# Kernel tuning notes

Measured on AMD Instinct MI355X. Metric: run time of the kernel, lower is better.

The kernel has to match this reference:

```python
import jax, jax.numpy as jnp
import numpy as np

B, CIN, COUT, H, W = 16, 512, 128, 64, 64


def setup_inputs() -> dict:
    key = jax.random.key(0)
    k1, k2, k3 = jax.random.split(key, 3)
    x = jax.random.normal(k1, (B, CIN, H, W), dtype=jnp.float32)
    style = jax.random.normal(k2, (B, CIN), dtype=jnp.float32)
    # kaiming_normal_ on [COUT, CIN, 1, 1]: fan_in = CIN*1*1, std = sqrt(2/fan_in)
    weight = jax.random.normal(k3, (COUT, CIN), dtype=jnp.float32) * np.float32(np.sqrt(2.0 / CIN))
    return {"x": x, "style": style, "weight": weight}


def reference(x, style, weight):
    # Per-sample modulated weight: mw[b,o,c] = style[b,c] * weight[o,c]
    # 1x1 conv, padding=0, stride=1 -> batched channel-mixing GEMM:
    # out[b,o,h,w] = sum_c mw[b,o,c] * x[b,c,h,w]
    return jnp.einsum('oc,bc,bchw->bohw', weight, style, x)
```

## Files before the change

### kernel.cpp

```cpp
#include <hip/hip_runtime.h>
#include <stdint.h>

#define NB    16
#define CIN   512
#define COUT  128
#define HW    4096
#define BN    128
#define BK    32
#define NIT   (CIN / BK)

using bf16x8  = __attribute__((ext_vector_type(8))) __bf16;
using floatx4 = __attribute__((ext_vector_type(4))) float;

__device__ __forceinline__ unsigned short f2bf_bits(float f) {
    union { float f; unsigned u; } v; v.f = f;
    return (unsigned short)((v.u + 0x7fffu + ((v.u >> 16) & 1u)) >> 16);
}

#define GLD16(g, l)                                                            \
    __builtin_amdgcn_global_load_lds(                                          \
        (const __attribute__((address_space(1))) void*)(g),                    \
        (__attribute__((address_space(3))) void*)(l), 16, 0, 0)

__global__ __launch_bounds__(256)
void modw_kernel(const float* __restrict__ style,
                 const float* __restrict__ weight,
                 __bf16* __restrict__ mw)
{
    const int id = blockIdx.x * 256 + threadIdx.x;
    const int k8 = id & 63;
    const int m  = (id >> 6) & 127;
    const int b  = id >> 13;

    const float4 w0 = *(const float4*)(weight + m * CIN + k8 * 8);
    const float4 w1 = *(const float4*)(weight + m * CIN + k8 * 8 + 4);
    const float4 s0 = *(const float4*)(style + b * CIN + k8 * 8);
    const float4 s1 = *(const float4*)(style + b * CIN + k8 * 8 + 4);

    union { unsigned short us[8]; bf16x8 v; } pk;
    pk.us[0] = f2bf_bits(w0.x * s0.x);
    pk.us[1] = f2bf_bits(w0.y * s0.y);
    pk.us[2] = f2bf_bits(w0.z * s0.z);
    pk.us[3] = f2bf_bits(w0.w * s0.w);
    pk.us[4] = f2bf_bits(w1.x * s1.x);
    pk.us[5] = f2bf_bits(w1.y * s1.y);
    pk.us[6] = f2bf_bits(w1.z * s1.z);
    pk.us[7] = f2bf_bits(w1.w * s1.w);
    *(bf16x8*)(mw + ((size_t)(b * 64 + k8) * 128 + m) * 8) = pk.v;
}

__global__ __launch_bounds__(512, 4)
void modconv1x1_kernel(const float* __restrict__ x,
                       const __bf16* __restrict__ mw,
                       float* __restrict__ out)
{
    __shared__ __align__(16) __bf16 Alds[2][4096];
    __shared__ __align__(16) __bf16 Bfs[2][4 * 128 * 8];

    const int tid  = threadIdx.x;
    const int lane = tid & 63;
    const int wave = tid >> 6;
    const int quad = lane >> 4;
    const int l15  = lane & 15;

    const int b  = blockIdx.x >> 5;
    const int n0 = (blockIdx.x & 31) * BN;

    float*       outb = out + (size_t)b * COUT * HW + n0;
    const char*  mwb  = (const char*)mw + (size_t)b * (64 * 128 * 16);

    const int wm = (wave & 1) * 64;
    const int wn = (wave >> 1) * 32;

    const int kg = tid >> 7;
    const int bn = tid & 127;
    const float* xbn = x + (size_t)b * CIN * HW + (size_t)kg * 8 * HW + n0 + bn;

    floatx4 acc[4][2];
    #pragma unroll
    for (int i = 0; i < 4; ++i)
        #pragma unroll
        for (int j = 0; j < 2; ++j)
            acc[i][j] = (floatx4){0.f, 0.f, 0.f, 0.f};

#define SISSUE(T, XR)                                                          \
    {                                                                          \
        const float* xp = xbn + (size_t)(T) * BK * HW;                         \
        _Pragma("unroll")                                                      \
        for (int j = 0; j < 8; ++j) XR[j] = xp[(size_t)j * HW];                \
    }

#define SWRITE(T, XR)                                                          \
    {                                                                          \
        union { unsigned short us[8]; bf16x8 v; } pk;                          \
        _Pragma("unroll")                                                      \
        for (int j = 0; j < 8; ++j) pk.us[j] = f2bf_bits(XR[j]);               \
        *(bf16x8*)&Bfs[(T) & 1][(kg * 128 + bn) * 8] = pk.v;                   \
    }

#define ADMA(T)                                                                \
    {                                                                          \
        const char* at = mwb + (size_t)(T) * 8192;                             \
        GLD16(at + wave * 1024 + lane * 16,                                    \
              (char*)&Alds[(T) & 1][0] + wave * 1024);                        \
    }

#define COMPUTE(BUF)                                                           \
    {                                                                          \
        bf16x8 af[4];                                                          \
        _Pragma("unroll")                                                      \
        for (int tm = 0; tm < 4; ++tm)                                         \
            af[tm] = *(const bf16x8*)&Alds[BUF][(quad * 128 + wm + tm * 16 + l15) * 8]; \
        bf16x8 bfr[2];                                                         \
        _Pragma("unroll")                                                      \
        for (int tn = 0; tn < 2; ++tn)                                         \
            bfr[tn] = *(const bf16x8*)&Bfs[BUF][(quad * 128 + wn + tn * 16 + l15) * 8]; \
        _Pragma("unroll")                                                      \
        for (int tm = 0; tm < 4; ++tm)                                         \
            _Pragma("unroll")                                                  \
            for (int tn = 0; tn < 2; ++tn)                                     \
                acc[tm][tn] = __builtin_amdgcn_mfma_f32_16x16x32_bf16(         \
                    af[tm], bfr[tn], acc[tm][tn], 0, 0, 0);                    \
    }

#define BODYF(IT, XC, XN)                                                      \
    {                                                                          \
        ADMA((IT) + 1)                                                         \
        COMPUTE((IT) & 1)                                                      \
        SISSUE((IT) + 2, XN)                                                   \
        SWRITE((IT) + 1, XC)                                                   \
        asm volatile("s_waitcnt vmcnt(8) lgkmcnt(0)" ::: "memory");            \
        __builtin_amdgcn_s_barrier();                                          \
    }

    float xa[8], xb[8];

    SISSUE(0, xa)
    ADMA(0)
    SWRITE(0, xa)
    SISSUE(1, xb)
    asm volatile("s_waitcnt vmcnt(8) lgkmcnt(0)" ::: "memory");
    __builtin_amdgcn_s_barrier();

    #pragma unroll 1
    for (int it2 = 0; it2 < 7; ++it2) {
        const int it = it2 * 2;
        BODYF(it,     xb, xa)
        BODYF(it + 1, xa, xb)
    }
    {
        ADMA(15)
        COMPUTE(0)
        SWRITE(15, xb)
        asm volatile("s_waitcnt vmcnt(0) lgkmcnt(0)" ::: "memory");
        __builtin_amdgcn_s_barrier();
    }
    COMPUTE(1)

#undef BODYF
#undef COMPUTE
#undef ADMA
#undef SWRITE
#undef SISSUE

    #pragma unroll
    for (int tm = 0; tm < 4; ++tm) {
        const int o = wm + tm * 16 + quad * 4;
        #pragma unroll
        for (int tn = 0; tn < 2; ++tn) {
            const int n = wn + tn * 16 + l15;
            #pragma unroll
            for (int r = 0; r < 4; ++r)
                outb[(size_t)(o + r) * HW + n] = acc[tm][tn][r];
        }
    }
}

extern "C" void kernel_launch(void* const* d_in, const int* in_sizes, int n_in,
                              void* d_out, int out_size, void* d_ws, size_t ws_size,
                              hipStream_t stream) {
    const float* x      = (const float*)d_in[0];
    const float* style  = (const float*)d_in[1];
    const float* weight = (const float*)d_in[2];
    float* out = (float*)d_out;
    __bf16* mw = (__bf16*)d_ws;

    modw_kernel<<<dim3(512), dim3(256), 0, stream>>>(style, weight, mw);
    modconv1x1_kernel<<<dim3(NB * 32), dim3(512), 0, stream>>>(x, mw, out);
}
```

Baseline: 205.8 us.

## Fuse style modulation into GEMM kernel, build A fragments in registers

```diff
diff --git a/kernel.cpp b/kernel.cpp
--- a/kernel.cpp
+++ b/kernel.cpp
@@ -17,44 +17,12 @@
     return (unsigned short)((v.u + 0x7fffu + ((v.u >> 16) & 1u)) >> 16);
 }
 
-#define GLD16(g, l)                                                            \
-    __builtin_amdgcn_global_load_lds(                                          \
-        (const __attribute__((address_space(1))) void*)(g),                    \
-        (__attribute__((address_space(3))) void*)(l), 16, 0, 0)
-
-__global__ __launch_bounds__(256)
-void modw_kernel(const float* __restrict__ style,
-                 const float* __restrict__ weight,
-                 __bf16* __restrict__ mw)
+__global__ __launch_bounds__(512, 4)
+void modconv_fused_kernel(const float* __restrict__ x,
+                          const float* __restrict__ style,
+                          const float* __restrict__ weight,
+                          float* __restrict__ out)
 {
-    const int id = blockIdx.x * 256 + threadIdx.x;
-    const int k8 = id & 63;
-    const int m  = (id >> 6) & 127;
-    const int b  = id >> 13;
-
-    const float4 w0 = *(const float4*)(weight + m * CIN + k8 * 8);
-    const float4 w1 = *(const float4*)(weight + m * CIN + k8 * 8 + 4);
-    const float4 s0 = *(const float4*)(style + b * CIN + k8 * 8);
-    const float4 s1 = *(const float4*)(style + b * CIN + k8 * 8 + 4);
-
-    union { unsigned short us[8]; bf16x8 v; } pk;
-    pk.us[0] = f2bf_bits(w0.x * s0.x);
-    pk.us[1] = f2bf_bits(w0.y * s0.y);
-    pk.us[2] = f2bf_bits(w0.z * s0.z);
-    pk.us[3] = f2bf_bits(w0.w * s0.w);
-    pk.us[4] = f2bf_bits(w1.x * s1.x);
-    pk.us[5] = f2bf_bits(w1.y * s1.y);
-    pk.us[6] = f2bf_bits(w1.z * s1.z);
-    pk.us[7] = f2bf_bits(w1.w * s1.w);
-    *(bf16x8*)(mw + ((size_t)(b * 64 + k8) * 128 + m) * 8) = pk.v;
-}
-
-__global__ __launch_bounds__(512, 4)
-void modconv1x1_kernel(const float* __restrict__ x,
-                       const __bf16* __restrict__ mw,
-                       float* __restrict__ out)
-{
-    __shared__ __align__(16) __bf16 Alds[2][4096];
     __shared__ __align__(16) __bf16 Bfs[2][4 * 128 * 8];
 
     const int tid  = threadIdx.x;
@@ -66,11 +34,16 @@
     const int b  = blockIdx.x >> 5;
     const int n0 = (blockIdx.x & 31) * BN;
 
-    float*       outb = out + (size_t)b * COUT * HW + n0;
-    const char*  mwb  = (const char*)mw + (size_t)b * (64 * 128 * 16);
+    float* outb = out + (size_t)b * COUT * HW + n0;
 
     const int wm = (wave & 1) * 64;
     const int wn = (wave >> 1) * 32;
+
+    const float* wr0 = weight + (size_t)(wm + 0 * 16 + l15) * CIN + quad * 8;
+    const float* wr1 = weight + (size_t)(wm + 1 * 16 + l15) * CIN + quad * 8;
+    const float* wr2 = weight + (size_t)(wm + 2 * 16 + l15) * CIN + quad * 8;
+    const float* wr3 = weight + (size_t)(wm + 3 * 16 + l15) * CIN + quad * 8;
+    const float* sb  = style + (size_t)b * CIN + quad * 8;
 
     const int kg = tid >> 7;
     const int bn = tid & 127;
@@ -82,6 +55,42 @@
         #pragma unroll
         for (int j = 0; j < 2; ++j)
             acc[i][j] = (floatx4){0.f, 0.f, 0.f, 0.f};
+
+    float4 sv0, sv1, w00, w01, w10, w11, w20, w21, w30, w31;
+    bf16x8 af0, af1, af2, af3;
+    float xa[8], xb[8];
+
+#define WLOAD(T)                                                               \
+    {                                                                          \
+        const int ko = (T) * BK;                                               \
+        sv0 = *(const float4*)(sb + ko);  sv1 = *(const float4*)(sb + ko + 4); \
+        w00 = *(const float4*)(wr0 + ko); w01 = *(const float4*)(wr0 + ko + 4);\
+        w10 = *(const float4*)(wr1 + ko); w11 = *(const float4*)(wr1 + ko + 4);\
+        w20 = *(const float4*)(wr2 + ko); w21 = *(const float4*)(wr2 + ko + 4);\
+        w30 = *(const float4*)(wr3 + ko); w31 = *(const float4*)(wr3 + ko + 4);\
+    }
+
+#define ABUILD()                                                               \
+    {                                                                          \
+        union { unsigned short us[8]; bf16x8 v; } p0, p1, p2, p3;              \
+        p0.us[0] = f2bf_bits(w00.x * sv0.x); p0.us[1] = f2bf_bits(w00.y * sv0.y); \
+        p0.us[2] = f2bf_bits(w00.z * sv0.z); p0.us[3] = f2bf_bits(w00.w * sv0.w); \
+        p0.us[4] = f2bf_bits(w01.x * sv1.x); p0.us[5] = f2bf_bits(w01.y * sv1.y); \
+        p0.us[6] = f2bf_bits(w01.z * sv1.z); p0.us[7] = f2bf_bits(w01.w * sv1.w); \
+        p1.us[0] = f2bf_bits(w10.x * sv0.x); p1.us[1] = f2bf_bits(w10.y * sv0.y); \
+        p1.us[2] = f2bf_bits(w10.z * sv0.z); p1.us[3] = f2bf_bits(w10.w * sv0.w); \
+        p1.us[4] = f2bf_bits(w11.x * sv1.x); p1.us[5] = f2bf_bits(w11.y * sv1.y); \
+        p1.us[6] = f2bf_bits(w11.z * sv1.z); p1.us[7] = f2bf_bits(w11.w * sv1.w); \
+        p2.us[0] = f2bf_bits(w20.x * sv0.x); p2.us[1] = f2bf_bits(w20.y * sv0.y); \
+        p2.us[2] = f2bf_bits(w20.z * sv0.z); p2.us[3] = f2bf_bits(w20.w * sv0.w); \
+        p2.us[4] = f2bf_bits(w21.x * sv1.x); p2.us[5] = f2bf_bits(w21.y * sv1.y); \
+        p2.us[6] = f2bf_bits(w21.z * sv1.z); p2.us[7] = f2bf_bits(w21.w * sv1.w); \
+        p3.us[0] = f2bf_bits(w30.x * sv0.x); p3.us[1] = f2bf_bits(w30.y * sv0.y); \
+        p3.us[2] = f2bf_bits(w30.z * sv0.z); p3.us[3] = f2bf_bits(w30.w * sv0.w); \
+        p3.us[4] = f2bf_bits(w31.x * sv1.x); p3.us[5] = f2bf_bits(w31.y * sv1.y); \
+        p3.us[6] = f2bf_bits(w31.z * sv1.z); p3.us[7] = f2bf_bits(w31.w * sv1.w); \
+        af0 = p0.v; af1 = p1.v; af2 = p2.v; af3 = p3.v;                        \
+    }
 
 #define SISSUE(T, XR)                                                          \
     {                                                                          \
@@ -98,70 +107,63 @@
         *(bf16x8*)&Bfs[(T) & 1][(kg * 128 + bn) * 8] = pk.v;                   \
     }
 
-#define ADMA(T)                                                                \
+#define COMPUTE(BUF)                                                           \
     {                                                                          \
-        const char* at = mwb + (size_t)(T) * 8192;                             \
-        GLD16(at + wave * 1024 + lane * 16,                                    \
-              (char*)&Alds[(T) & 1][0] + wave * 1024);                        \
+        bf16x8 bfr0 = *(const bf16x8*)&Bfs[BUF][(quad * 128 + wn + l15) * 8];  \
+        bf16x8 bfr1 = *(const bf16x8*)&Bfs[BUF][(quad * 128 + wn + 16 + l15) * 8]; \
+        acc[0][0] = __builtin_amdgcn_mfma_f32_16x16x32_bf16(af0, bfr0, acc[0][0], 0, 0, 0); \
+        acc[0][1] = __builtin_amdgcn_mfma_f32_16x16x32_bf16(af0, bfr1, acc[0][1], 0, 0, 0); \
+        acc[1][0] = __builtin_amdgcn_mfma_f32_16x16x32_bf16(af1, bfr0, acc[1][0], 0, 0, 0); \
+        acc[1][1] = __builtin_amdgcn_mfma_f32_16x16x32_bf16(af1, bfr1, acc[1][1], 0, 0, 0); \
+        acc[2][0] = __builtin_amdgcn_mfma_f32_16x16x32_bf16(af2, bfr0, acc[2][0], 0, 0, 0); \
+        acc[2][1] = __builtin_amdgcn_mfma_f32_16x16x32_bf16(af2, bfr1, acc[2][1], 0, 0, 0); \
+        acc[3][0] = __builtin_amdgcn_mfma_f32_16x16x32_bf16(af3, bfr0, acc[3][0], 0, 0, 0); \
+        acc[3][1] = __builtin_amdgcn_mfma_f32_16x16x32_bf16(af3, bfr1, acc[3][1], 0, 0, 0); \
     }
 
-#define COMPUTE(BUF)                                                           \
+#define BODY(IT, XC, XN)                                                       \
     {                                                                          \
-        bf16x8 af[4];                                                          \
-        _Pragma("unroll")                                                      \
-        for (int tm = 0; tm < 4; ++tm)                                         \
-            af[tm] = *(const bf16x8*)&Alds[BUF][(quad * 128 + wm + tm * 16 + l15) * 8]; \
-        bf16x8 bfr[2];                                                         \
-        _Pragma("unroll")                                                      \
-        for (int tn = 0; tn < 2; ++tn)                                         \
-            bfr[tn] = *(const bf16x8*)&Bfs[BUF][(quad * 128 + wn + tn * 16 + l15) * 8]; \
-        _Pragma("unroll")                                                      \
-        for (int tm = 0; tm < 4; ++tm)                                         \
-            _Pragma("unroll")                                                  \
-            for (int tn = 0; tn < 2; ++tn)                                     \
-                acc[tm][tn] = __builtin_amdgcn_mfma_f32_16x16x32_bf16(         \
-                    af[tm], bfr[tn], acc[tm][tn], 0, 0, 0);                    \
-    }
-
-#define BODYF(IT, XC, XN)                                                      \
-    {                                                                          \
-        ADMA((IT) + 1)                                                         \
+        ABUILD()                                                               \
+        WLOAD((IT) + 1)                                                        \
         COMPUTE((IT) & 1)                                                      \
         SISSUE((IT) + 2, XN)                                                   \
         SWRITE((IT) + 1, XC)                                                   \
-        asm volatile("s_waitcnt vmcnt(8) lgkmcnt(0)" ::: "memory");            \
+        asm volatile("s_waitcnt lgkmcnt(0)" ::: "memory");                     \
         __builtin_amdgcn_s_barrier();                                          \
     }
 
-    float xa[8], xb[8];
-
+    WLOAD(0)
     SISSUE(0, xa)
-    ADMA(0)
     SWRITE(0, xa)
     SISSUE(1, xb)
-    asm volatile("s_waitcnt vmcnt(8) lgkmcnt(0)" ::: "memory");
+    asm volatile("s_waitcnt lgkmcnt(0)" ::: "memory");
     __builtin_amdgcn_s_barrier();
 
     #pragma unroll 1
     for (int it2 = 0; it2 < 7; ++it2) {
         const int it = it2 * 2;
-        BODYF(it,     xb, xa)
-        BODYF(it + 1, xa, xb)
+        BODY(it,     xb, xa)
+        BODY(it + 1, xa, xb)
     }
     {
-        ADMA(15)
+        ABUILD()
+        WLOAD(15)
         COMPUTE(0)
         SWRITE(15, xb)
-        asm volatile("s_waitcnt vmcnt(0) lgkmcnt(0)" ::: "memory");
+        asm volatile("s_waitcnt lgkmcnt(0)" ::: "memory");
         __builtin_amdgcn_s_barrier();
     }
-    COMPUTE(1)
+    {
+        ABUILD()
+        COMPUTE(1)
+    }
 
-#undef BODYF
+#undef BODY
 #undef COMPUTE
-#undef ADMA
 #undef SWRITE
 #undef SISSUE
+#undef ABUILD
+#undef WLOAD
 
     #pragma unroll
     for (int tm = 0; tm < 4; ++tm) {
@@ -183,8 +185,7 @@
     const float* style  = (const float*)d_in[1];
     const float* weight = (const float*)d_in[2];
     float* out = (float*)d_out;
-    __bf16* mw = (__bf16*)d_ws;
+    (void)d_ws; (void)ws_size;
 
-    modw_kernel<<<dim3(512), dim3(256), 0, stream>>>(style, weight, mw);
-    modconv1x1_kernel<<<dim3(NB * 32), dim3(512), 0, stream>>>(x, mw, out);
+    modconv_fused_kernel<<<dim3(NB * 32), dim3(512), 0, stream>>>(x, style, weight, out);
 }
```

New measurement: 265.9 us. +29.2%, slower.

## Fuse weight modulation into the conv GEMM kernel, dropping the prep kernel

Applied to the files above, without the earlier changes.

```diff
diff --git a/kernel.cpp b/kernel.cpp
--- a/kernel.cpp
+++ b/kernel.cpp
@@ -17,44 +17,13 @@
     return (unsigned short)((v.u + 0x7fffu + ((v.u >> 16) & 1u)) >> 16);
 }
 
-#define GLD16(g, l)                                                            \
-    __builtin_amdgcn_global_load_lds(                                          \
-        (const __attribute__((address_space(1))) void*)(g),                    \
-        (__attribute__((address_space(3))) void*)(l), 16, 0, 0)
-
-__global__ __launch_bounds__(256)
-void modw_kernel(const float* __restrict__ style,
-                 const float* __restrict__ weight,
-                 __bf16* __restrict__ mw)
+__global__ __launch_bounds__(512, 4)
+void modconv_fused_kernel(const float* __restrict__ x,
+                          const float* __restrict__ style,
+                          const float* __restrict__ weight,
+                          float* __restrict__ out)
 {
-    const int id = blockIdx.x * 256 + threadIdx.x;
-    const int k8 = id & 63;
-    const int m  = (id >> 6) & 127;
-    const int b  = id >> 13;
-
-    const float4 w0 = *(const float4*)(weight + m * CIN + k8 * 8);
-    const float4 w1 = *(const float4*)(weight + m * CIN + k8 * 8 + 4);
-    const float4 s0 = *(const float4*)(style + b * CIN + k8 * 8);
-    const float4 s1 = *(const float4*)(style + b * CIN + k8 * 8 + 4);
-
-    union { unsigned short us[8]; bf16x8 v; } pk;
-    pk.us[0] = f2bf_bits(w0.x * s0.x);
-    pk.us[1] = f2bf_bits(w0.y * s0.y);
-    pk.us[2] = f2bf_bits(w0.z * s0.z);
-    pk.us[3] = f2bf_bits(w0.w * s0.w);
-    pk.us[4] = f2bf_bits(w1.x * s1.x);
-    pk.us[5] = f2bf_bits(w1.y * s1.y);
-    pk.us[6] = f2bf_bits(w1.z * s1.z);
-    pk.us[7] = f2bf_bits(w1.w * s1.w);
-    *(bf16x8*)(mw + ((size_t)(b * 64 + k8) * 128 + m) * 8) = pk.v;
-}
-
-__global__ __launch_bounds__(512, 4)
-void modconv1x1_kernel(const float* __restrict__ x,
-                       const __bf16* __restrict__ mw,
-                       float* __restrict__ out)
-{
-    __shared__ __align__(16) __bf16 Alds[2][4096];
+    __shared__ __align__(16) __bf16 Alds[2][4 * 128 * 8];
     __shared__ __align__(16) __bf16 Bfs[2][4 * 128 * 8];
 
     const int tid  = threadIdx.x;
@@ -66,11 +35,16 @@
     const int b  = blockIdx.x >> 5;
     const int n0 = (blockIdx.x & 31) * BN;
 
-    float*       outb = out + (size_t)b * COUT * HW + n0;
-    const char*  mwb  = (const char*)mw + (size_t)b * (64 * 128 * 16);
+    float* outb = out + (size_t)b * COUT * HW + n0;
 
     const int wm = (wave & 1) * 64;
     const int wn = (wave >> 1) * 32;
+
+    const int am  = tid >> 2;
+    const int ak8 = tid & 3;
+    const float* wrow = weight + (size_t)am * CIN + ak8 * 8;
+    const float* srow = style + (size_t)b * CIN + ak8 * 8;
+    const int aoff = (ak8 * 128 + am) * 8;
 
     const int kg = tid >> 7;
     const int bn = tid & 127;
@@ -82,6 +56,27 @@
         #pragma unroll
         for (int j = 0; j < 2; ++j)
             acc[i][j] = (floatx4){0.f, 0.f, 0.f, 0.f};
+
+    float  xa[8], xb[8];
+    float4 wa0, wa1, sa0, sa1;
+    float4 wb0, wb1, sb0, sb1;
+
+#define WISSUE(T, W0, W1, S0, S1)                                              \
+    {                                                                          \
+        const int ko = (T) * BK;                                               \
+        W0 = *(const float4*)(wrow + ko); W1 = *(const float4*)(wrow + ko + 4);\
+        S0 = *(const float4*)(srow + ko); S1 = *(const float4*)(srow + ko + 4);\
+    }
+
+#define AWRITE(T, W0, W1, S0, S1)                                              \
+    {                                                                          \
+        union { unsigned short us[8]; bf16x8 v; } pk;                          \
+        pk.us[0] = f2bf_bits(W0.x * S0.x); pk.us[1] = f2bf_bits(W0.y * S0.y);  \
+        pk.us[2] = f2bf_bits(W0.z * S0.z); pk.us[3] = f2bf_bits(W0.w * S0.w);  \
+        pk.us[4] = f2bf_bits(W1.x * S1.x); pk.us[5] = f2bf_bits(W1.y * S1.y);  \
+        pk.us[6] = f2bf_bits(W1.z * S1.z); pk.us[7] = f2bf_bits(W1.w * S1.w);  \
+        *(bf16x8*)&Alds[(T) & 1][aoff] = pk.v;                                 \
+    }
 
 #define SISSUE(T, XR)                                                          \
     {                                                                          \
@@ -96,13 +91,6 @@
         _Pragma("unroll")                                                      \
         for (int j = 0; j < 8; ++j) pk.us[j] = f2bf_bits(XR[j]);               \
         *(bf16x8*)&Bfs[(T) & 1][(kg * 128 + bn) * 8] = pk.v;                   \
-    }
-
-#define ADMA(T)                                                                \
-    {                                                                          \
-        const char* at = mwb + (size_t)(T) * 8192;                             \
-        GLD16(at + wave * 1024 + lane * 16,                                    \
-              (char*)&Alds[(T) & 1][0] + wave * 1024);                        \
     }
 
 #define COMPUTE(BUF)                                                           \
@@ -123,45 +111,47 @@
                     af[tm], bfr[tn], acc[tm][tn], 0, 0, 0);                    \
     }
 
-#define BODYF(IT, XC, XN)                                                      \
+#define BODY(IT, XC, XN, WC0, WC1, SC0, SC1, WN0, WN1, SN0, SN1)               \
     {                                                                          \
-        ADMA((IT) + 1)                                                         \
         COMPUTE((IT) & 1)                                                      \
+        WISSUE((IT) + 2, WN0, WN1, SN0, SN1)                                   \
         SISSUE((IT) + 2, XN)                                                   \
+        AWRITE((IT) + 1, WC0, WC1, SC0, SC1)                                   \
         SWRITE((IT) + 1, XC)                                                   \
-        asm volatile("s_waitcnt vmcnt(8) lgkmcnt(0)" ::: "memory");            \
+        asm volatile("s_waitcnt lgkmcnt(0)" ::: "memory");                     \
         __builtin_amdgcn_s_barrier();                                          \
     }
 
-    float xa[8], xb[8];
-
+    WISSUE(0, wa0, wa1, sa0, sa1)
     SISSUE(0, xa)
-    ADMA(0)
+    AWRITE(0, wa0, wa1, sa0, sa1)
     SWRITE(0, xa)
+    WISSUE(1, wb0, wb1, sb0, sb1)
     SISSUE(1, xb)
-    asm volatile("s_waitcnt vmcnt(8) lgkmcnt(0)" ::: "memory");
+    asm volatile("s_waitcnt lgkmcnt(0)" ::: "memory");
     __builtin_amdgcn_s_barrier();
 
     #pragma unroll 1
     for (int it2 = 0; it2 < 7; ++it2) {
         const int it = it2 * 2;
-        BODYF(it,     xb, xa)
-        BODYF(it + 1, xa, xb)
+        BODY(it,     xb, xa, wb0, wb1, sb0, sb1, wa0, wa1, sa0, sa1)
+        BODY(it + 1, xa, xb, wa0, wa1, sa0, sa1, wb0, wb1, sb0, sb1)
     }
     {
-        ADMA(15)
         COMPUTE(0)
+        AWRITE(15, wb0, wb1, sb0, sb1)
         SWRITE(15, xb)
-        asm volatile("s_waitcnt vmcnt(0) lgkmcnt(0)" ::: "memory");
+        asm volatile("s_waitcnt lgkmcnt(0)" ::: "memory");
         __builtin_amdgcn_s_barrier();
     }
     COMPUTE(1)
 
-#undef BODYF
+#undef BODY
 #undef COMPUTE
-#undef ADMA
 #undef SWRITE
 #undef SISSUE
+#undef AWRITE
+#undef WISSUE
 
     #pragma unroll
     for (int tm = 0; tm < 4; ++tm) {
@@ -183,8 +173,7 @@
     const float* style  = (const float*)d_in[1];
     const float* weight = (const float*)d_in[2];
     float* out = (float*)d_out;
-    __bf16* mw = (__bf16*)d_ws;
+    (void)d_ws; (void)ws_size;
 
-    modw_kernel<<<dim3(512), dim3(256), 0, stream>>>(style, weight, mw);
-    modconv1x1_kernel<<<dim3(NB * 32), dim3(512), 0, stream>>>(x, mw, out);
+    modconv_fused_kernel<<<dim3(NB * 32), dim3(512), 0, stream>>>(x, style, weight, out);
 }
```

Result: no change. 203.9 us (-0.9%).
